# Performance work log

Hardware: AMD Instinct MI355X
Metric: run time of the kernel (lower is better)

## Reference

```python
import jax, jax.numpy as jnp
import numpy as np

N = 64            # HiPPO order
DT = 1.0 / 512.0  # discretization timestep ~ 1/seq_len


def _hippo_legt_discrete(n, dt):
    """Continuous HiPPO-LegT (A,B) then bilinear (Tustin) discretization,
    matching scipy.signal.cont2discrete(..., method='bilinear')."""
    Q = np.arange(n, dtype=np.float64)
    R = (2 * Q + 1)[:, None]
    j, i = np.meshgrid(Q, Q)
    A = np.where(i < j, -1.0, (-1.0) ** (i - j + 1)) * R
    B = (-1.0) ** Q[:, None] * R  # (n, 1)
    I = np.eye(n)
    ima = I - (dt / 2.0) * A
    Ad = np.linalg.solve(ima, I + (dt / 2.0) * A)
    Bd = np.linalg.solve(ima, dt * B).squeeze(-1)  # (n,)
    return Ad, Bd


def setup_inputs() -> dict:
    key = jax.random.key(0)
    inputs = jax.random.normal(key, (16, 128, 512), dtype=jnp.float32)  # (b, d, L)
    Ad, Bd = _hippo_legt_discrete(N, DT)
    return {
        "inputs": inputs,
        "A": jnp.asarray(Ad, dtype=jnp.float32),  # (N, N)
        "B": jnp.asarray(Bd, dtype=jnp.float32),  # (N,)
    }


def reference(inputs, A, B):
    # inputs: (b, d, L) -> iterate over last axis, state c: (b, d, N)
    fs = jnp.moveaxis(inputs, -1, 0)  # (L, b, d)
    c0 = jnp.zeros(inputs.shape[:-1] + (A.shape[0],), dtype=inputs.dtype)

    def step(c, f):
        # c_t = c_{t-1} @ A^T + f_t[..., None] * B   (F.linear(c, A) == c @ A^T)
        c_new = c @ A.T + f[..., None] * B
        return c_new, c_new

    _, cs = jax.lax.scan(step, c0, fs)
    return cs  # (L, b, d, N)
```

## Files before the change

### kernel.cpp

```cpp
#include <hip/hip_runtime.h>


typedef _Float16 half8  __attribute__((ext_vector_type(8)));
typedef float    f32x4  __attribute__((ext_vector_type(4)));

#define SEQN 2048
#define LT   512

typedef const __attribute__((address_space(1))) unsigned int kGU32;
typedef __attribute__((address_space(3))) unsigned int kLU32;

__device__ __forceinline__ void cp16(const void* g, void* l) {
  __builtin_amdgcn_global_load_lds((kGU32*)g, (kLU32*)l, 16, 0, 0);
}

__device__ __forceinline__ void mul64(const float* XT, const float* Y,
                                      float* outT, float* outN, int t) {
  const int r = (t >> 5) * 4;
  const int c = (t & 31) * 2;
  float a00 = 0.f, a01 = 0.f, a10 = 0.f, a11 = 0.f;
  float a20 = 0.f, a21 = 0.f, a30 = 0.f, a31 = 0.f;
#pragma unroll 4
  for (int l = 0; l < 64; ++l) {
    const float4 x = *(const float4*)(XT + l * 64 + r);
    const float2 y = *(const float2*)(Y + l * 64 + c);
    a00 += x.x * y.x; a01 += x.x * y.y;
    a10 += x.y * y.x; a11 += x.y * y.y;
    a20 += x.z * y.x; a21 += x.z * y.y;
    a30 += x.w * y.x; a31 += x.w * y.y;
  }
  __syncthreads();
  if (outT) {
    outT[(c + 0) * 64 + r + 0] = a00; outT[(c + 1) * 64 + r + 0] = a01;
    outT[(c + 0) * 64 + r + 1] = a10; outT[(c + 1) * 64 + r + 1] = a11;
    outT[(c + 0) * 64 + r + 2] = a20; outT[(c + 1) * 64 + r + 2] = a21;
    outT[(c + 0) * 64 + r + 3] = a30; outT[(c + 1) * 64 + r + 3] = a31;
  }
  if (outN) {
    outN[(r + 0) * 64 + c + 0] = a00; outN[(r + 0) * 64 + c + 1] = a01;
    outN[(r + 1) * 64 + c + 0] = a10; outN[(r + 1) * 64 + c + 1] = a11;
    outN[(r + 2) * 64 + c + 0] = a20; outN[(r + 2) * 64 + c + 1] = a21;
    outN[(r + 3) * 64 + c + 0] = a30; outN[(r + 3) * 64 + c + 1] = a31;
  }
  __syncthreads();
}

__global__ __launch_bounds__(512) void squares_fh(
    const float* __restrict__ A, const float* __restrict__ f,
    float* __restrict__ SqT, _Float16* __restrict__ fh_t) {
  __shared__ float S[4096];
  __shared__ float STr[4096];
  const int t = threadIdx.x;
  if (blockIdx.x == 0) {
    for (int i = t; i < 4096; i += 512) {
      const float v = A[i];
      S[i] = v;
      STr[(i & 63) * 64 + (i >> 6)] = v;
    }
    __syncthreads();
    for (int i = t; i < 4096; i += 512) SqT[i] = STr[i];
    for (int k = 1; k < 9; ++k) {
      mul64(STr, S, STr, S, t);
      for (int i = t; i < 4096; i += 512) SqT[k * 4096 + i] = STr[i];
    }
  } else {
    const int g = (blockIdx.x - 1) * 512 + t;
    const int row = g >> 6, kc = g & 63;
    const float4* s = (const float4*)(f + (size_t)row * LT + kc * 8);
    const float4 a = s[0], b = s[1];
    half8 v;
    v[0] = (_Float16)a.x; v[1] = (_Float16)a.y;
    v[2] = (_Float16)a.z; v[3] = (_Float16)a.w;
    v[4] = (_Float16)b.x; v[5] = (_Float16)b.y;
    v[6] = (_Float16)b.z; v[7] = (_Float16)b.w;
    const int off = ((row >> 4) * 16 + (kc >> 2)) * 512 + (row & 15) * 32 +
                    (kc & 3) * 8;
    *(half8*)(fh_t + off) = v;
  }
}

__global__ __launch_bounds__(512) void kvec_fill(
    const float* __restrict__ SqT, const float* __restrict__ B,
    _Float16* __restrict__ Lc) {
  __shared__ float Kb[8][64];
  const int t = threadIdx.x;
  const int b = blockIdx.x;

  {
    const int ch = b * 512 + t;
    const int c = ch >> 12, n = (ch >> 6) & 63, zc = ch & 63;
    const uint4 zz = {0u, 0u, 0u, 0u};
    *(uint4*)(Lc + (size_t)c * 65536 + n * 1024 + 512 + zc * 8) = zz;
  }
  if (b == 0) {
    for (int e = t; e < 1792; e += 512) {
      int e2 = e, c = 1;
      while (e2 >= 64 * c) { e2 -= 64 * c; ++c; }
      const int n = e2 & 63, dz = e2 >> 6;
      Lc[(size_t)c * 65536 + n * 1024 + (512 - c + dz)] = (_Float16)0.f;
    }
  }

  const int g = t >> 6, n = t & 63;
  const int i = b * 8 + g;
  float kreg = B[n];
  for (int k = 0; k < 9; ++k) {
    Kb[g][n] = kreg;
    __syncthreads();
    if ((i >> k) & 1) {
      const float* Sk = SqT + k * 4096 + n;
      float s = 0.f;
#pragma unroll 16
      for (int m = 0; m < 64; ++m) s += Sk[m * 64] * Kb[g][m];
      kreg = s;
    }
    __syncthreads();
  }
#pragma unroll
  for (int c = 0; c < 8; ++c) {
    const int z = 511 - i - c;
    if (z >= 0) Lc[(size_t)c * 65536 + n * 1024 + z] = (_Float16)kreg;
  }
}

__global__ __launch_bounds__(256) void causal_gemm(
    const _Float16* __restrict__ fh_t, const _Float16* __restrict__ Lc,
    float* __restrict__ out) {
  __shared__ _Float16 Ws[128 * 64];

  const int tid = threadIdx.x;
  const int bn = 255 - (int)blockIdx.x;
  const int bm = blockIdx.y;
  const int lane = tid & 63, wid = tid >> 6;
  const int wm = wid >> 1, wn = wid & 1;
  const int l15 = lane & 15, quad = lane >> 4;
  const int needK = 2 * bn + 2;
  const int KH = (needK + 63) >> 6;

  const int srow = lane >> 3;
  const int jp = (lane & 7) ^ srow;

  const _Float16* wp[4];
  int ldso[4];
#pragma unroll
  for (int q = 0; q < 4; ++q) {
    const int rl = wid * 32 + q * 8 + srow;
    const int tau = 2 * bn + (rl >> 6);
    const int n = rl & 63;
    const int o0 = 511 - tau;
    const int c = o0 & 7;
    wp[q] = Lc + (size_t)c * 65536 + n * 1024 + (o0 - c) + jp * 8;
    ldso[q] = (wid * 32 + q * 8) * 64;
  }

  const _Float16* px =
      fh_t + (size_t)(bm * 8 + wm * 4) * 8192 + l15 * 32 + quad * 8;

  f32x4 acc[4][4];
  const f32x4 z4 = {0.f, 0.f, 0.f, 0.f};
#pragma unroll
  for (int i = 0; i < 4; ++i)
#pragma unroll
    for (int j = 0; j < 4; ++j) acc[i][j] = z4;

  for (int kh = 0; kh < KH; ++kh) {
    if (kh) __syncthreads();
    const size_t go = (size_t)kh * 64;
#pragma unroll
    for (int q = 0; q < 4; ++q) cp16(wp[q] + go, &Ws[ldso[q]]);
    __syncthreads();

#pragma unroll
    for (int kk = 0; kk < 2; ++kk) {
      if (kh * 64 + kk * 32 < needK) {
        half8 av[4], bv[4];
#pragma unroll
        for (int fm = 0; fm < 4; ++fm)
          av[fm] = *(const half8*)(px + fm * 8192 + (kh * 2 + kk) * 512);
#pragma unroll
        for (int fn = 0; fn < 4; ++fn) {
          const int r = wn * 64 + fn * 16 + l15;
          bv[fn] = *(const half8*)&Ws[r * 64 +
                                      (((kk * 4 + quad) ^ (l15 & 7)) << 3)];
        }
#pragma unroll
        for (int fm = 0; fm < 4; ++fm)
#pragma unroll
          for (int fn = 0; fn < 4; ++fn)
            acc[fm][fn] = __builtin_amdgcn_mfma_f32_16x16x32_f16(
                av[fm], bv[fn], acc[fm][fn], 0, 0, 0);
      }
    }
  }

  const int taug = bn * 2 + wn;
#pragma unroll
  for (int fm = 0; fm < 4; ++fm) {
#pragma unroll
    for (int rr = 0; rr < 4; ++rr) {
      const size_t row =
          (size_t)taug * SEQN + (bm * 128 + wm * 64 + fm * 16 + quad * 4 + rr);
      float* o = out + row * 64 + l15;
#pragma unroll
      for (int fn = 0; fn < 4; ++fn) o[fn * 16] = acc[fm][fn][rr];
    }
  }
}

extern "C" void kernel_launch(void* const* d_in, const int* in_sizes, int n_in,
                              void* d_out, int out_size, void* d_ws,
                              size_t ws_size, hipStream_t stream) {
  const float* f = (const float*)d_in[0];
  const float* A = (const float*)d_in[1];
  const float* B = (const float*)d_in[2];
  float* out = (float*)d_out;

  _Float16* Lc = (_Float16*)d_ws;
  float* SqT = (float*)((char*)d_ws + (1 << 20));
  _Float16* fh_t =
      (_Float16*)((char*)d_ws + (1 << 20) + (192 << 10));

  squares_fh<<<257, 512, 0, stream>>>(A, f, SqT, fh_t);
  kvec_fill<<<64, 512, 0, stream>>>(SqT, B, Lc);
  causal_gemm<<<dim3(256, 16), 256, 0, stream>>>(fh_t, Lc, out);
}
```

Baseline: 326.4 us.

## Pre-tile Toeplitz kernel into MFMA fragment layout and drop LDS staging

Adds a wt_fill kernel that expands the per-tau kernel vectors into a fully materialised, fragment-ordered fp16 weight tensor. The GEMM can then load B operands directly from global memory, without LDS staging, shared-memory swizzles or barriers. The grid is reshaped so each block handles two M tiles in sequence, which reuses the per-tau weights across passes. In exchange it writes and reads a much larger weight buffer (about 32 MB of workspace) and adds an extra kernel launch.

```diff
diff --git a/kernel.cpp b/kernel.cpp
--- a/kernel.cpp
+++ b/kernel.cpp
@@ -6,13 +6,6 @@
 
 #define SEQN 2048
 #define LT   512
-
-typedef const __attribute__((address_space(1))) unsigned int kGU32;
-typedef __attribute__((address_space(3))) unsigned int kLU32;
-
-__device__ __forceinline__ void cp16(const void* g, void* l) {
-  __builtin_amdgcn_global_load_lds((kGU32*)g, (kLU32*)l, 16, 0, 0);
-}
 
 __device__ __forceinline__ void mul64(const float* XT, const float* Y,
                                       float* outT, float* outN, int t) {
@@ -81,26 +74,10 @@
 
 __global__ __launch_bounds__(512) void kvec_fill(
     const float* __restrict__ SqT, const float* __restrict__ B,
-    _Float16* __restrict__ Lc) {
+    float* __restrict__ Lf) {
   __shared__ float Kb[8][64];
   const int t = threadIdx.x;
   const int b = blockIdx.x;
-
-  {
-    const int ch = b * 512 + t;
-    const int c = ch >> 12, n = (ch >> 6) & 63, zc = ch & 63;
-    const uint4 zz = {0u, 0u, 0u, 0u};
-    *(uint4*)(Lc + (size_t)c * 65536 + n * 1024 + 512 + zc * 8) = zz;
-  }
-  if (b == 0) {
-    for (int e = t; e < 1792; e += 512) {
-      int e2 = e, c = 1;
-      while (e2 >= 64 * c) { e2 -= 64 * c; ++c; }
-      const int n = e2 & 63, dz = e2 >> 6;
-      Lc[(size_t)c * 65536 + n * 1024 + (512 - c + dz)] = (_Float16)0.f;
-    }
-  }
-
   const int g = t >> 6, n = t & 63;
   const int i = b * 8 + g;
   float kreg = B[n];
@@ -116,93 +93,82 @@
     }
     __syncthreads();
   }
+  Lf[n * 512 + 511 - i] = kreg;
+}
+
+__global__ __launch_bounds__(256) void wt_fill(const float* __restrict__ Lf,
+                                               _Float16* __restrict__ Wt) {
+  const int b = blockIdx.x;
+  const int tau = b >> 4, kq = b & 15;
+  if (kq * 32 > tau) return;
+  const int t = threadIdx.x;
+  const int fn = t >> 6, c = t & 63;
+  const int l15 = c >> 2, quad = c & 3;
+  const int n = fn * 16 + l15;
+  const int o = 511 - tau + kq * 32 + quad * 8;
+  const float* src = Lf + n * 512;
+  half8 v;
 #pragma unroll
-  for (int c = 0; c < 8; ++c) {
-    const int z = 511 - i - c;
-    if (z >= 0) Lc[(size_t)c * 65536 + n * 1024 + z] = (_Float16)kreg;
+  for (int u = 0; u < 8; ++u) {
+    const int z = o + u;
+    v[u] = (z < 512) ? (_Float16)src[z] : (_Float16)0.f;
   }
+  *(half8*)(Wt + ((size_t)(tau * 4 + fn) * 16 + kq) * 512 + l15 * 32 +
+            quad * 8) = v;
 }
 
 __global__ __launch_bounds__(256) void causal_gemm(
-    const _Float16* __restrict__ fh_t, const _Float16* __restrict__ Lc,
+    const _Float16* __restrict__ fh_t, const _Float16* __restrict__ Wt,
     float* __restrict__ out) {
-  __shared__ _Float16 Ws[128 * 64];
-
-  const int tid = threadIdx.x;
-  const int bn = 255 - (int)blockIdx.x;
-  const int bm = blockIdx.y;
-  const int lane = tid & 63, wid = tid >> 6;
+  const int bmp = blockIdx.x;
+  const int bn = 255 - (int)blockIdx.y;
+  const int lane = threadIdx.x & 63, wid = threadIdx.x >> 6;
   const int wm = wid >> 1, wn = wid & 1;
   const int l15 = lane & 15, quad = lane >> 4;
-  const int needK = 2 * bn + 2;
-  const int KH = (needK + 63) >> 6;
+  const int tau = 2 * bn + wn;
+  const int KQ = (tau >> 5) + 1;
+  const int lo = l15 * 32 + quad * 8;
 
-  const int srow = lane >> 3;
-  const int jp = (lane & 7) ^ srow;
-
-  const _Float16* wp[4];
-  int ldso[4];
-#pragma unroll
-  for (int q = 0; q < 4; ++q) {
-    const int rl = wid * 32 + q * 8 + srow;
-    const int tau = 2 * bn + (rl >> 6);
-    const int n = rl & 63;
-    const int o0 = 511 - tau;
-    const int c = o0 & 7;
-    wp[q] = Lc + (size_t)c * 65536 + n * 1024 + (o0 - c) + jp * 8;
-    ldso[q] = (wid * 32 + q * 8) * 64;
-  }
-
-  const _Float16* px =
-      fh_t + (size_t)(bm * 8 + wm * 4) * 8192 + l15 * 32 + quad * 8;
-
-  f32x4 acc[4][4];
-  const f32x4 z4 = {0.f, 0.f, 0.f, 0.f};
-#pragma unroll
-  for (int i = 0; i < 4; ++i)
-#pragma unroll
-    for (int j = 0; j < 4; ++j) acc[i][j] = z4;
-
-  for (int kh = 0; kh < KH; ++kh) {
-    if (kh) __syncthreads();
-    const size_t go = (size_t)kh * 64;
-#pragma unroll
-    for (int q = 0; q < 4; ++q) cp16(wp[q] + go, &Ws[ldso[q]]);
-    __syncthreads();
+  const _Float16* pw = Wt + (size_t)tau * 64 * 512 + lo;
 
 #pragma unroll
-    for (int kk = 0; kk < 2; ++kk) {
-      if (kh * 64 + kk * 32 < needK) {
-        half8 av[4], bv[4];
+  for (int pass = 0; pass < 2; ++pass) {
+    const int bm = bmp * 2 + pass;
+    const _Float16* px = fh_t + (size_t)(bm * 8 + wm * 4) * 8192 + lo;
+
+    f32x4 acc[4][4];
+    const f32x4 z4 = {0.f, 0.f, 0.f, 0.f};
 #pragma unroll
-        for (int fm = 0; fm < 4; ++fm)
-          av[fm] = *(const half8*)(px + fm * 8192 + (kh * 2 + kk) * 512);
+    for (int i = 0; i < 4; ++i)
 #pragma unroll
-        for (int fn = 0; fn < 4; ++fn) {
-          const int r = wn * 64 + fn * 16 + l15;
-          bv[fn] = *(const half8*)&Ws[r * 64 +
-                                      (((kk * 4 + quad) ^ (l15 & 7)) << 3)];
-        }
+      for (int j = 0; j < 4; ++j) acc[i][j] = z4;
+
+    for (int kq = 0; kq < KQ; ++kq) {
+      half8 av[4], bv[4];
 #pragma unroll
-        for (int fm = 0; fm < 4; ++fm)
+      for (int fm = 0; fm < 4; ++fm)
+        av[fm] = *(const half8*)(px + fm * 8192 + kq * 512);
 #pragma unroll
-          for (int fn = 0; fn < 4; ++fn)
-            acc[fm][fn] = __builtin_amdgcn_mfma_f32_16x16x32_f16(
-                av[fm], bv[fn], acc[fm][fn], 0, 0, 0);
+      for (int fn = 0; fn < 4; ++fn)
+        bv[fn] = *(const half8*)(pw + (fn * 16 + kq) * 512);
+#pragma unroll
+      for (int fm = 0; fm < 4; ++fm)
+#pragma unroll
+        for (int fn = 0; fn < 4; ++fn)
+          acc[fm][fn] = __builtin_amdgcn_mfma_f32_16x16x32_f16(
+              av[fm], bv[fn], acc[fm][fn], 0, 0, 0);
+    }
+
+#pragma unroll
+    for (int fm = 0; fm < 4; ++fm) {
+#pragma unroll
+      for (int rr = 0; rr < 4; ++rr) {
+        const size_t row = (size_t)tau * SEQN +
+                           (bm * 128 + wm * 64 + fm * 16 + quad * 4 + rr);
+        float* o = out + row * 64 + l15;
+#pragma unroll
+        for (int fn = 0; fn < 4; ++fn) o[fn * 16] = acc[fm][fn][rr];
       }
-    }
-  }
-
-  const int taug = bn * 2 + wn;
-#pragma unroll
-  for (int fm = 0; fm < 4; ++fm) {
-#pragma unroll
-    for (int rr = 0; rr < 4; ++rr) {
-      const size_t row =
-          (size_t)taug * SEQN + (bm * 128 + wm * 64 + fm * 16 + quad * 4 + rr);
-      float* o = out + row * 64 + l15;
-#pragma unroll
-      for (int fn = 0; fn < 4; ++fn) o[fn * 16] = acc[fm][fn][rr];
     }
   }
 }
@@ -215,12 +181,14 @@
   const float* B = (const float*)d_in[2];
   float* out = (float*)d_out;
 
-  _Float16* Lc = (_Float16*)d_ws;
-  float* SqT = (float*)((char*)d_ws + (1 << 20));
-  _Float16* fh_t =
-      (_Float16*)((char*)d_ws + (1 << 20) + (192 << 10));
+  _Float16* Wt = (_Float16*)d_ws;
+  char* p = (char*)d_ws + (32 << 20);
+  float* Lf = (float*)p;
+  float* SqT = (float*)(p + (128 << 10));
+  _Float16* fh_t = (_Float16*)(p + (320 << 10));
 
   squares_fh<<<257, 512, 0, stream>>>(A, f, SqT, fh_t);
-  kvec_fill<<<64, 512, 0, stream>>>(SqT, B, Lc);
-  causal_gemm<<<dim3(256, 16), 256, 0, stream>>>(fh_t, Lc, out);
+  kvec_fill<<<64, 512, 0, stream>>>(SqT, B, Lf);
+  wt_fill<<<8192, 256, 0, stream>>>(Lf, Wt);
+  causal_gemm<<<dim3(8, 256), 256, 0, stream>>>(fh_t, Wt, out);
 }
```

Result: slower. 375.5 us (+15.0%).
